# Kernel optimization log

Measured on AMD Instinct MI355X. Metric: run time of the kernel, lower is better.

The kernel has to match this reference:

```python
import jax, jax.numpy as jnp
import numpy as np

B, S, HID = 2, 2048, 2048
H, KVH, D = 32, 4, 128
EPS = 1e-6
ROPE_THETA = 1e6
INIT = 0.02


def setup_inputs() -> dict:
    key = jax.random.key(0)
    ks = jax.random.split(key, 6)
    hidden_states = jax.random.normal(ks[0], (B, S, HID), jnp.float32)
    q_w = jax.random.normal(ks[1], (HID, H * D), jnp.float32) * INIT
    k_w = jax.random.normal(ks[2], (HID, KVH * D), jnp.float32) * INIT
    v_w = jax.random.normal(ks[3], (HID, KVH * D), jnp.float32) * INIT
    o_w = jax.random.normal(ks[4], (H * D, HID), jnp.float32) * INIT
    q_norm_w = jnp.ones((D,), jnp.float32)
    k_norm_w = jnp.ones((D,), jnp.float32)
    # rotary embeddings, computed once per position (B, S, D)
    pos = jnp.arange(S, dtype=jnp.float32)
    inv_freq = 1.0 / (ROPE_THETA ** (jnp.arange(0, D, 2, dtype=jnp.float32) / D))
    freqs = pos[:, None] * inv_freq[None, :]          # (S, D/2)
    emb = jnp.concatenate([freqs, freqs], axis=-1)    # (S, D)
    cos = jnp.broadcast_to(jnp.cos(emb)[None], (B, S, D))
    sin = jnp.broadcast_to(jnp.sin(emb)[None], (B, S, D))
    # causal mask (is_causal=True, sliding_window=None)
    attn_mask = jnp.tril(jnp.ones((S, S), bool))[None, None]  # (1,1,S,S)
    return {"hidden_states": hidden_states, "cos": cos, "sin": sin,
            "q_w": q_w, "k_w": k_w, "v_w": v_w, "o_w": o_w,
            "q_norm_w": q_norm_w, "k_norm_w": k_norm_w, "attn_mask": attn_mask}


def _rms_norm(x, w):
    xf = x.astype(jnp.float32)
    var = jnp.mean(jax.lax.square(xf), axis=-1, keepdims=True)
    return (w * (xf * jax.lax.rsqrt(var + EPS))).astype(x.dtype)


def _rotate_half(x):
    x1, x2 = jnp.split(x, 2, axis=-1)
    return jnp.concatenate([-x2, x1], axis=-1)


def _apply_rope(q, k, cos, sin):
    # q: (B,H,S,D), k: (B,KVH,S,D); cos/sin: (B,S,D) -> (B,1,S,D)
    cos = cos[:, None]
    sin = sin[:, None]
    q = q * cos + _rotate_half(q) * sin
    k = k * cos + _rotate_half(k) * sin
    return q, k


def reference(hidden_states, cos, sin, q_w, k_w, v_w, o_w, q_norm_w, k_norm_w, attn_mask):
    b, s, _ = hidden_states.shape
    scaling = D ** (-0.5)
    # projections + per-head QK RMSNorm
    q = _rms_norm((hidden_states @ q_w).reshape(b, s, H, D), q_norm_w)
    k = _rms_norm((hidden_states @ k_w).reshape(b, s, KVH, D), k_norm_w)
    v = (hidden_states @ v_w).reshape(b, s, KVH, D)
    q = jnp.transpose(q, (0, 2, 1, 3))   # (b,H,s,D)
    k = jnp.transpose(k, (0, 2, 1, 3))   # (b,KVH,s,D)
    v = jnp.transpose(v, (0, 2, 1, 3))
    q, k = _apply_rope(q, k, cos, sin)
    # GQA: repeat KV heads across groups
    groups = H // KVH
    k = jnp.repeat(k, groups, axis=1)    # (b,H,s,D)
    v = jnp.repeat(v, groups, axis=1)
    # eager softmax attention (fp32 softmax)
    scores = jnp.einsum('bhqd,bhkd->bhqk', q, k).astype(jnp.float32) * scaling
    scores = jnp.where(attn_mask, scores, jnp.float32(-1e30))
    probs = jax.nn.softmax(scores, axis=-1).astype(q.dtype)
    attn = jnp.einsum('bhqk,bhkd->bhqd', probs, v)
    attn = jnp.transpose(attn, (0, 2, 1, 3)).reshape(b, s, H * D)
    return attn @ o_w
```

## Files before the change

### kernel.cpp

```cpp
#include <hip/hip_runtime.h>
#include <hip/hip_bf16.h>

typedef unsigned short u16;
typedef __attribute__((ext_vector_type(4))) float f32x4;
typedef __attribute__((ext_vector_type(16))) float f32x16;
typedef __attribute__((ext_vector_type(8))) short bf16x8;
typedef __attribute__((ext_vector_type(4))) unsigned u32x4;

#define B_ 2
#define S_ 2048
#define HID_ 2048
#define H_ 32
#define KVH_ 4
#define D_ 128
#define M_ 4096
#define NQ_ 4096
#define NKV_ 512

typedef const __attribute__((address_space(1))) void gconst_void;
typedef __attribute__((address_space(3))) void lds_void;

static __device__ __forceinline__ void gload_lds16(const void* g, void* l) {
  __builtin_amdgcn_global_load_lds((gconst_void*)g, (lds_void*)l, 16, 0, 0);
}

#define WAITV(N) asm volatile("s_waitcnt vmcnt(" #N ")" ::: "memory")
#define WAITL0() asm volatile("s_waitcnt lgkmcnt(0)" ::: "memory")
#define SBAR() __builtin_amdgcn_s_barrier()
#define SCHED0() __builtin_amdgcn_sched_barrier(0)
#define CFENCE() asm volatile("" ::: "memory")

static __device__ __forceinline__ u16 f2b(float f) {
  union { float f; unsigned i; } x; x.f = f;
  return (u16)((x.i + 0x7fffu + ((x.i >> 16) & 1u)) >> 16);
}
static __device__ __forceinline__ float b2f(u16 u) {
  union { unsigned i; float f; } x; x.i = ((unsigned)u) << 16;
  return x.f;
}
static __device__ __forceinline__ float max3f(float a, float b, float c) {
  float d;
  asm("v_max3_f32 %0, %1, %2, %3" : "=v"(d) : "v"(a), "v"(b), "v"(c));
  return d;
}

static __device__ __forceinline__ void tr_tile(const float* __restrict__ W,
    u16* __restrict__ Wt, int K, int N, int n0, int k0, u16 (*t)[72]) {
  int tid = threadIdx.x;
  int r = tid >> 4;
  int c4 = (tid & 15) * 4;
#pragma unroll
  for (int i = 0; i < 4; i++) {
    int k = r + i * 16;
    float4 v = *reinterpret_cast<const float4*>(W + (size_t)(k0 + k) * N + n0 + c4);
    t[k][c4 + 0] = f2b(v.x); t[k][c4 + 1] = f2b(v.y);
    t[k][c4 + 2] = f2b(v.z); t[k][c4 + 3] = f2b(v.w);
  }
  __syncthreads();
#pragma unroll
  for (int i = 0; i < 4; i++) {
    int n = r + i * 16;
    ushort4 o;
    o.x = t[c4 + 0][n]; o.y = t[c4 + 1][n]; o.z = t[c4 + 2][n]; o.w = t[c4 + 3][n];
    *reinterpret_cast<ushort4*>(Wt + (size_t)(n0 + n) * K + k0 + c4) = o;
  }
}

__global__ __launch_bounds__(256) void k_prep(const float* __restrict__ hidden, u16* __restrict__ hb,
    const float* __restrict__ qw, u16* __restrict__ qwt,
    const float* __restrict__ kw, u16* __restrict__ kwt,
    const float* __restrict__ vw, u16* __restrict__ vwt,
    const float* __restrict__ ow, u16* __restrict__ owt) {
  __shared__ u16 t[64][72];
  const int bid = blockIdx.x;
  if (bid < 2048) {
    const int n4 = M_ * HID_ / 4;
    int i = bid * 256 + threadIdx.x;
    const int stride = 2048 * 256;
    for (; i < n4; i += stride) {
      float4 v = reinterpret_cast<const float4*>(hidden)[i];
      ushort4 o;
      o.x = f2b(v.x); o.y = f2b(v.y); o.z = f2b(v.z); o.w = f2b(v.w);
      reinterpret_cast<ushort4*>(hb)[i] = o;
    }
  } else if (bid < 4096) {
    int l = bid - 2048;
    tr_tile(qw, qwt, HID_, NQ_, (l & 63) * 64, (l >> 6) * 64, t);
  } else if (bid < 4352) {
    int l = bid - 4096;
    tr_tile(kw, kwt, HID_, NKV_, (l & 7) * 64, (l >> 3) * 64, t);
  } else if (bid < 4608) {
    int l = bid - 4352;
    tr_tile(vw, vwt, HID_, NKV_, (l & 7) * 64, (l >> 3) * 64, t);
  } else {
    int l = bid - 4608;
    tr_tile(ow, owt, NQ_, HID_, (l & 31) * 64, (l >> 5) * 64, t);
  }
}

__device__ __forceinline__ void gemm_core(const u16* __restrict__ A, const u16* __restrict__ Bt,
                                          int K, int m0, int n0,
                                          u16* As, u16* Bs, f32x4 (&acc)[4][4]) {
  const int tid = threadIdx.x;
  const int lane = tid & 63;
  const int wid = tid >> 6;
  const int wr = wid >> 1, wc = wid & 1;
  const int lrow = lane & 15;
  const int hi = lane >> 4;
  const f32x4 zz = {0.f, 0.f, 0.f, 0.f};
#pragma unroll
  for (int i = 0; i < 4; i++)
#pragma unroll
    for (int j = 0; j < 4; j++) acc[i][j] = zz;

  const int srow = tid >> 3;
  const int sc16 = tid & 7;
  const int nk = K >> 6;
  int cur = 0;

#pragma unroll
  for (int rep = 0; rep < 4; rep++) {
    int row = rep * 32 + srow;
    int gcol = ((sc16 ^ (row & 7)) << 3);
    gload_lds16(A + (size_t)(m0 + row) * K + gcol, As + row * 64 + sc16 * 8);
    gload_lds16(Bt + (size_t)(n0 + row) * K + gcol, Bs + row * 64 + sc16 * 8);
  }

  for (int t = 0; t < nk; t++) {
    if (t + 1 < nk) {
      int nxt = cur ^ 1;
      int kb = (t + 1) << 6;
#pragma unroll
      for (int rep = 0; rep < 4; rep++) {
        int row = rep * 32 + srow;
        int gcol = kb + ((sc16 ^ (row & 7)) << 3);
        gload_lds16(A + (size_t)(m0 + row) * K + gcol, As + nxt * 8192 + row * 64 + sc16 * 8);
        gload_lds16(Bt + (size_t)(n0 + row) * K + gcol, Bs + nxt * 8192 + row * 64 + sc16 * 8);
      }
      WAITV(8);
    } else {
      WAITV(0);
    }
    SCHED0(); SBAR(); CFENCE(); SCHED0();

    const u16* Ac = As + cur * 8192;
    const u16* Bc = Bs + cur * 8192;
#pragma unroll
    for (int kc = 0; kc < 2; kc++) {
      bf16x8 af[4], bfr[4];
#pragma unroll
      for (int i = 0; i < 4; i++) {
        int row = wr * 64 + i * 16 + lrow;
        af[i] = *reinterpret_cast<const bf16x8*>(Ac + row * 64 + ((((kc << 2) + hi) ^ (row & 7)) << 3));
      }
#pragma unroll
      for (int j = 0; j < 4; j++) {
        int row = wc * 64 + j * 16 + lrow;
        bfr[j] = *reinterpret_cast<const bf16x8*>(Bc + row * 64 + ((((kc << 2) + hi) ^ (row & 7)) << 3));
      }
#pragma unroll
      for (int i = 0; i < 4; i++)
#pragma unroll
        for (int j = 0; j < 4; j++)
          acc[i][j] = __builtin_amdgcn_mfma_f32_16x16x32_bf16(af[i], bfr[j], acc[i][j], 0, 0, 0);
    }
    SBAR(); SCHED0();
    cur ^= 1;
  }
}

__global__ __launch_bounds__(512, 2) void k_gemm_q8(const u16* __restrict__ A,
    const u16* __restrict__ Bt, u16* __restrict__ qb) {
  __shared__ u16 Ash[2][2][128 * 64];
  __shared__ u16 Bsh[2][2][128 * 64];
  const int bid = blockIdx.x;
  const int wg = (bid & 7) * 32 + (bid >> 3);
  const int mt = wg & 15, nt = wg >> 4;
  const int m0 = mt * 256, n0 = nt * 256;
  const int K = HID_, nk = K >> 6;
  const int tid = threadIdx.x, lane = tid & 63;
  const int wv = tid >> 6, wr = wv >> 2, wc = wv & 3;
  const int lrow = lane & 15, hi4 = lane >> 4;

  const int s0r = tid >> 3, sc = tid & 7;
  const int s1r = (tid + 512) >> 3;

  auto stgA = [&](int h, int t, int d) {
    gload_lds16(A + (size_t)(m0 + h * 128 + s0r) * K + t * 64 + ((sc ^ (s0r & 7)) << 3),
                &Ash[d][h][s0r * 64 + sc * 8]);
    gload_lds16(A + (size_t)(m0 + h * 128 + s1r) * K + t * 64 + ((sc ^ (s1r & 7)) << 3),
                &Ash[d][h][s1r * 64 + sc * 8]);
  };
  auto stgB = [&](int h, int t, int d) {
    gload_lds16(Bt + (size_t)(n0 + h * 128 + s0r) * K + t * 64 + ((sc ^ (s0r & 7)) << 3),
                &Bsh[d][h][s0r * 64 + sc * 8]);
    gload_lds16(Bt + (size_t)(n0 + h * 128 + s1r) * K + t * 64 + ((sc ^ (s1r & 7)) << 3),
                &Bsh[d][h][s1r * 64 + sc * 8]);
  };

  f32x4 acc[8][4];
  const f32x4 zz = {0.f, 0.f, 0.f, 0.f};
#pragma unroll
  for (int f = 0; f < 8; f++)
#pragma unroll
    for (int j = 0; j < 4; j++) acc[f][j] = zz;

  bf16x8 af0[4][2], af1[4][2], bfr[2][2];

  auto lda = [&](bf16x8 (&dst)[4][2], int mh, int d) {
#pragma unroll
    for (int fi = 0; fi < 4; fi++) {
      int row = fi * 32 + wr * 16 + lrow;
#pragma unroll
      for (int kk = 0; kk < 2; kk++)
        dst[fi][kk] = *reinterpret_cast<const bf16x8*>(
            &Ash[d][mh][row * 64 + ((((kk << 2) + hi4) ^ (row & 7)) << 3)]);
    }
  };
  auto ldb = [&](int nh, int d) {
#pragma unroll
    for (int ji = 0; ji < 2; ji++) {
      int row = ji * 64 + wc * 16 + lrow;
#pragma unroll
      for (int kk = 0; kk < 2; kk++)
        bfr[ji][kk] = *reinterpret_cast<const bf16x8*>(
            &Bsh[d][nh][row * 64 + ((((kk << 2) + hi4) ^ (row & 7)) << 3)]);
    }
  };
  auto mq = [&](bf16x8 (&afh)[4][2], int mh, int nh) {
    __builtin_amdgcn_s_setprio(1);
#pragma unroll
    for (int kk = 0; kk < 2; kk++)
#pragma unroll
      for (int fi = 0; fi < 4; fi++)
#pragma unroll
        for (int ji = 0; ji < 2; ji++)
          acc[mh * 4 + fi][nh * 2 + ji] = __builtin_amdgcn_mfma_f32_16x16x32_bf16(
              afh[fi][kk], bfr[ji][kk], acc[mh * 4 + fi][nh * 2 + ji], 0, 0, 0);
    __builtin_amdgcn_s_setprio(0);
  };

  stgA(0, 0, 0); stgA(1, 0, 0); stgB(0, 0, 0); stgB(1, 0, 0);
  WAITV(2); SCHED0();
  SBAR(); SCHED0();

  for (int t = 0; t < nk; t++) {
    const int d = t & 1, nd = d ^ 1;
    const bool pre = (t + 1 < nk);
    lda(af0, 0, d); ldb(0, d);
    if (pre) stgA(0, t + 1, nd);
    SCHED0(); SBAR();
    WAITL0(); SCHED0();
    mq(af0, 0, 0);
    SBAR(); SCHED0();
    lda(af1, 1, d);
    if (pre) stgA(1, t + 1, nd);
    WAITV(4); SCHED0(); SBAR();
    WAITL0(); SCHED0();
    mq(af1, 1, 0);
    SBAR(); SCHED0();
    ldb(1, d);
    if (pre) stgB(0, t + 1, nd);
    SCHED0(); SBAR();
    WAITL0(); SCHED0();
    mq(af1, 1, 1);
    SBAR(); SCHED0();
    if (pre) stgB(1, t + 1, nd);
    WAITV(2); SCHED0(); SBAR();
    mq(af0, 0, 1);
    SBAR(); SCHED0();
  }

  const int lr4 = hi4 * 4, lc = lane & 15;
#pragma unroll
  for (int f = 0; f < 8; f++)
#pragma unroll
    for (int j = 0; j < 4; j++)
#pragma unroll
      for (int rr = 0; rr < 4; rr++) {
        int m = m0 + f * 32 + wr * 16 + lr4 + rr;
        int ncol = n0 + j * 64 + wc * 16 + lc;
        int b = m >> 11, s = m & (S_ - 1);
        int head = ncol >> 7, dd = ncol & 127;
        qb[(((size_t)b * H_ + head) * S_ + s) * D_ + dd] = f2b(acc[f][j][rr]);
      }
}

__global__ __launch_bounds__(256, 2) void k_gemm_kv(const u16* __restrict__ hb,
    const u16* __restrict__ kwt, const u16* __restrict__ vwt,
    u16* __restrict__ kb, u16* __restrict__ vb) {
  __shared__ u16 As[2 * 128 * 64], Bs[2 * 128 * 64];
  const int bid = blockIdx.x;
  const int wg = (bid & 7) * 32 + (bid >> 3);
  const int mt = wg & 31, nt = wg >> 5;
  const bool isv = nt >= 4;
  const int head = isv ? nt - 4 : nt;
  const u16* Bt = isv ? vwt : kwt;
  f32x4 acc[4][4];
  gemm_core(hb, Bt, HID_, mt * 128, head * 128, As, Bs, acc);
  const int lane = threadIdx.x & 63;
  const int wid = threadIdx.x >> 6;
  const int wr = wid >> 1, wc = wid & 1;
  const int lr4 = (lane >> 4) * 4, lc = lane & 15;
#pragma unroll
  for (int i = 0; i < 4; i++)
#pragma unroll
    for (int j = 0; j < 4; j++)
#pragma unroll
      for (int r = 0; r < 4; r++) {
        int m = mt * 128 + wr * 64 + i * 16 + lr4 + r;
        int d = wc * 64 + j * 16 + lc;
        int b = m >> 11, s = m & (S_ - 1);
        u16 val = f2b(acc[i][j][r]);
        if (isv) vb[(((size_t)b * KVH_ + head) * D_ + d) * S_ + s] = val;
        else     kb[(((size_t)b * KVH_ + head) * S_ + s) * D_ + d] = val;
      }
}

__global__ __launch_bounds__(256, 2) void k_gemm_o(const u16* __restrict__ ab,
    const u16* __restrict__ owt, float* __restrict__ out) {
  __shared__ u16 As[2 * 128 * 64], Bs[2 * 128 * 64];
  const int bid = blockIdx.x;
  const int wg = (bid & 7) * 64 + (bid >> 3);
  const int mt = wg & 31, nt = wg >> 5;
  f32x4 acc[4][4];
  gemm_core(ab, owt, NQ_, mt * 128, nt * 128, As, Bs, acc);
  const int lane = threadIdx.x & 63;
  const int wid = threadIdx.x >> 6;
  const int wr = wid >> 1, wc = wid & 1;
  const int lr4 = (lane >> 4) * 4, lc = lane & 15;
#pragma unroll
  for (int i = 0; i < 4; i++)
#pragma unroll
    for (int j = 0; j < 4; j++)
#pragma unroll
      for (int r = 0; r < 4; r++) {
        int m = mt * 128 + wr * 64 + i * 16 + lr4 + r;
        int n = nt * 128 + wc * 64 + j * 16 + lc;
        out[(size_t)m * HID_ + n] = acc[i][j][r];
      }
}

__global__ __launch_bounds__(256) void k_norm_rope(u16* __restrict__ qb, u16* __restrict__ kb,
    const float* __restrict__ cosp, const float* __restrict__ sinp,
    const float* __restrict__ qnw, const float* __restrict__ knw) {
  int row = blockIdx.x * 4 + (threadIdx.x >> 6);
  int lane = threadIdx.x & 63;
  const int QROWS = B_ * H_ * S_;
  u16* ptr; const float* nw; int b, s; float os;
  if (row < QROWS) {
    ptr = qb + (size_t)row * D_; nw = qnw;
    s = row & (S_ - 1); b = row / (H_ * S_);
    os = 0.08838834764831845f * 1.44269504088896340f;
  } else {
    int r2 = row - QROWS;
    ptr = kb + (size_t)r2 * D_; nw = knw;
    s = r2 & (S_ - 1); b = r2 / (KVH_ * S_);
    os = 1.0f;
  }
  int d = lane * 2;
  float x0 = b2f(ptr[d]), x1 = b2f(ptr[d + 1]);
  float ss = x0 * x0 + x1 * x1;
#pragma unroll
  for (int m = 1; m < 64; m <<= 1) ss += __shfl_xor(ss, m);
  float inv = rsqrtf(ss * (1.0f / 128.0f) + 1e-6f) * os;
  x0 = x0 * inv * nw[d]; x1 = x1 * inv * nw[d + 1];
  float p0 = __shfl_xor(x0, 32), p1 = __shfl_xor(x1, 32);
  float r0 = (lane < 32) ? -p0 : p0;
  float r1 = (lane < 32) ? -p1 : p1;
  const float* cp = cosp + ((size_t)b * S_ + s) * D_;
  const float* sp = sinp + ((size_t)b * S_ + s) * D_;
  ptr[d]     = f2b(x0 * cp[d]     + r0 * sp[d]);
  ptr[d + 1] = f2b(x1 * cp[d + 1] + r1 * sp[d + 1]);
}

__global__ __launch_bounds__(256, 2) void k_attn(const u16* __restrict__ q,
    const u16* __restrict__ k, const u16* __restrict__ vt, u16* __restrict__ out) {
  __shared__ u16 Kb[2 * 64 * 128];
  __shared__ u16 Vb[128 * 64];
  const int bid = blockIdx.x;
  const int wg = (bid & 7) * 64 + (bid >> 3);
  const int qx = wg & 7, bh = wg >> 3;
  const int b = bh >> 5, h = bh & 31;
  const int kvh = h >> 3;
  const int tid = threadIdx.x, lane = tid & 63, w = tid >> 6;
  const int lq = lane & 31, hi = lane >> 5;
  const u16* qp  = q  + ((size_t)(b * H_ + h) * S_) * D_;
  const u16* kp  = k  + ((size_t)(b * KVH_ + kvh) * S_) * D_;
  const u16* vtp = vt + ((size_t)(b * KVH_ + kvh) * D_) * S_;

  const int rowKa = tid >> 4;
  const int colK  = ((tid & 15) ^ (rowKa & 15)) << 3;
  const int rowVa = tid >> 3;
  const int colV  = ((tid & 7) ^ (rowVa & 7)) << 3;

  auto stageK = [&](int n0, int cu) {
    u16* kd = Kb + cu * 8192 + tid * 8;
#pragma unroll
    for (int p = 0; p < 4; p++)
      gload_lds16(kp + (size_t)(n0 + p * 16 + rowKa) * D_ + colK, kd + p * 2048);
  };
  auto stageV = [&](int n0) {
    u16* vd = Vb + tid * 8;
#pragma unroll
    for (int p = 0; p < 4; p++)
      gload_lds16(vtp + (size_t)(p * 32 + rowVa) * S_ + n0 + colV, vd + p * 2048);
  };

  const f32x16 z16 = {0.f};
  int cur = 0;

  for (int half = 0; half < 2; half++) {
    const int qt = half ? (15 - qx) : qx;
    const int q0 = qt * 128;
    const int last = 2 * qt + 1;
    const int qg = q0 + 32 * w + lq;

    SBAR(); SCHED0();
    stageK(0, cur);
    stageV(0);

    bf16x8 qf[8];
#pragma unroll
    for (int ds = 0; ds < 8; ds++)
      qf[ds] = *reinterpret_cast<const bf16x8*>(qp + (size_t)qg * D_ + ds * 16 + hi * 8);

    f32x16 oacc[4];
#pragma unroll
    for (int dt = 0; dt < 4; dt++) oacc[dt] = z16;
    float mrun = -1e30f, lrun = 0.f;

    for (int nt = 0; nt <= last; nt++) {
      const int n0 = nt * 64;
      if (nt < last) {
        stageK(n0 + 64, cur ^ 1);
        WAITV(8);
      } else {
        WAITV(4);
      }
      SCHED0(); SBAR(); CFENCE(); SCHED0();

      const u16* Kc = Kb + cur * 8192;
      const bool skip = (n0 > q0 + 32 * w + 31);

      f32x16 sacc[2];
      if (!skip) {
        const bool needmask = (n0 + 63 > q0 + 32 * w);

        sacc[0] = z16; sacc[1] = z16;
#pragma unroll
        for (int ds = 0; ds < 8; ds++) {
          const int sl = (((ds << 1) + hi) ^ (lq & 15)) << 3;
          bf16x8 ka0 = *reinterpret_cast<const bf16x8*>(Kc + lq * 128 + sl);
          bf16x8 ka1 = *reinterpret_cast<const bf16x8*>(Kc + (lq + 32) * 128 + sl);
          __builtin_amdgcn_s_setprio(1);
          sacc[0] = __builtin_amdgcn_mfma_f32_32x32x16_bf16(ka0, qf[ds], sacc[0], 0, 0, 0);
          sacc[1] = __builtin_amdgcn_mfma_f32_32x32x16_bf16(ka1, qf[ds], sacc[1], 0, 0, 0);
          __builtin_amdgcn_s_setprio(0);
        }

        if (needmask) {
#pragma unroll
          for (int t = 0; t < 2; t++)
#pragma unroll
            for (int r = 0; r < 16; r++) {
              int kvg = n0 + 32 * t + (r & 3) + 8 * (r >> 2) + 4 * hi;
              if (kvg > qg) sacc[t][r] = -1e30f;
            }
        }
        float tm = fmaxf(sacc[0][0], sacc[0][1]);
#pragma unroll
        for (int i = 1; i < 16; i++) {
          const int e0 = 2 * i, e1 = 2 * i + 1;
          tm = max3f(tm, sacc[e0 >> 4][e0 & 15], sacc[e1 >> 4][e1 & 15]);
        }
        tm = fmaxf(tm, __shfl_xor(tm, 32));
        if (__any(tm > mrun + 8.f)) {
          float mn = fmaxf(mrun, tm);
          float al = exp2f(mrun - mn);
          mrun = mn;
          lrun *= al;
#pragma unroll
          for (int r = 0; r < 16; r++) {
            float ar = __shfl(al, (r & 3) + 8 * (r >> 2) + 4 * hi);
#pragma unroll
            for (int dt = 0; dt < 4; dt++) oacc[dt][r] *= ar;
          }
        }
        float rs = 0.f;
#pragma unroll
        for (int t = 0; t < 2; t++)
#pragma unroll
          for (int r = 0; r < 16; r++) {
            float pv = exp2f(sacc[t][r] - mrun);
            sacc[t][r] = pv;
            rs += pv;
          }
        rs += __shfl_xor(rs, 32);
        lrun += rs;
      }

      if (nt < last) WAITV(4); else WAITV(0);
      SCHED0(); SBAR(); CFENCE(); SCHED0();

      if (!skip) {
        u32x4 pa[4];
#pragma unroll
        for (int t = 0; t < 2; t++)
#pragma unroll
          for (int ksl = 0; ksl < 2; ksl++) {
            unsigned wa, wb, wc2, wd;
            asm("v_cvt_pk_bf16_f32 %0, %1, %2" : "=v"(wa)
                : "v"(sacc[t][8 * ksl + 0]), "v"(sacc[t][8 * ksl + 1]));
            asm("v_cvt_pk_bf16_f32 %0, %1, %2" : "=v"(wb)
                : "v"(sacc[t][8 * ksl + 2]), "v"(sacc[t][8 * ksl + 3]));
            asm("v_cvt_pk_bf16_f32 %0, %1, %2" : "=v"(wc2)
                : "v"(sacc[t][8 * ksl + 4]), "v"(sacc[t][8 * ksl + 5]));
            asm("v_cvt_pk_bf16_f32 %0, %1, %2" : "=v"(wd)
                : "v"(sacc[t][8 * ksl + 6]), "v"(sacc[t][8 * ksl + 7]));
            asm("v_permlane32_swap_b32 %0, %1" : "+v"(wa), "+v"(wc2));
            asm("v_permlane32_swap_b32 %0, %1" : "+v"(wb), "+v"(wd));
            u32x4 t4 = {wa, wb, wc2, wd};
            pa[t * 2 + ksl] = t4;
          }

#pragma unroll
        for (int ks = 0; ks < 4; ks++) {
          bf16x8 paf = __builtin_bit_cast(bf16x8, pa[ks]);
          bf16x8 bv[4];
#pragma unroll
          for (int dt = 0; dt < 4; dt++) {
            int rowv = dt * 32 + lq;
            bv[dt] = *reinterpret_cast<const bf16x8*>(
                Vb + rowv * 64 + ((((ks << 1) + hi) ^ (rowv & 7)) << 3));
          }
          __builtin_amdgcn_s_setprio(1);
#pragma unroll
          for (int dt = 0; dt < 4; dt++)
            oacc[dt] = __builtin_amdgcn_mfma_f32_32x32x16_bf16(paf, bv[dt], oacc[dt], 0, 0, 0);
          __builtin_amdgcn_s_setprio(0);
        }
      }

      if (nt < last) {
        SBAR(); SCHED0();
        stageV(nt * 64 + 64);
      }
      cur ^= 1;
    }

    float linv = 1.0f / lrun;
#pragma unroll
    for (int r = 0; r < 16; r++) {
      const int idx_r = (r & 3) + 8 * (r >> 2) + 4 * hi;
      float lr = __shfl(linv, idx_r);
      size_t base = ((size_t)b * S_ + (q0 + 32 * w + idx_r)) * NQ_ + h * D_ + lq;
#pragma unroll
      for (int dt = 0; dt < 4; dt++)
        out[base + dt * 32] = f2b(oacc[dt][r] * lr);
    }
  }
}

extern "C" void kernel_launch(void* const* d_in, const int* in_sizes, int n_in,
                              void* d_out, int out_size, void* d_ws, size_t ws_size,
                              hipStream_t stream) {
  const float* hidden = (const float*)d_in[0];
  const float* cosp   = (const float*)d_in[1];
  const float* sinp   = (const float*)d_in[2];
  const float* q_w    = (const float*)d_in[3];
  const float* k_w    = (const float*)d_in[4];
  const float* v_w    = (const float*)d_in[5];
  const float* o_w    = (const float*)d_in[6];
  const float* qnw    = (const float*)d_in[7];
  const float* knw    = (const float*)d_in[8];

  char* p = (char*)d_ws;
  u16* hb  = (u16*)p; p += (size_t)M_ * HID_ * 2;
  u16* qwt = (u16*)p; p += (size_t)NQ_ * HID_ * 2;
  u16* kwt = (u16*)p; p += (size_t)NKV_ * HID_ * 2;
  u16* vwt = (u16*)p; p += (size_t)NKV_ * HID_ * 2;
  u16* owt = (u16*)p; p += (size_t)HID_ * NQ_ * 2;
  u16* qb  = (u16*)p; p += (size_t)B_ * H_ * S_ * D_ * 2;
  u16* kb  = (u16*)p; p += (size_t)B_ * KVH_ * S_ * D_ * 2;
  u16* vb  = (u16*)p; p += (size_t)B_ * KVH_ * S_ * D_ * 2;
  u16* ab  = (u16*)p; p += (size_t)M_ * NQ_ * 2;

  k_prep<<<6656, 256, 0, stream>>>(hidden, hb, q_w, qwt, k_w, kwt, v_w, vwt, o_w, owt);
  k_gemm_q8<<<256, 512, 0, stream>>>(hb, qwt, qb);
  k_gemm_kv<<<256, 256, 0, stream>>>(hb, kwt, vwt, kb, vb);
  k_norm_rope<<<(B_ * H_ * S_ + B_ * KVH_ * S_) / 4, 256, 0, stream>>>(qb, kb, cosp, sinp, qnw, knw);
  k_attn<<<512, 256, 0, stream>>>(qb, kb, vb, ab);
  k_gemm_o<<<512, 256, 0, stream>>>(ab, owt, (float*)d_out);
}
```

Baseline: 319.0 us.

## Use 256x128 8-wave O-projection GEMM and one query tile per attention block

Replaces the 128x128 O-projection GEMM with a 512-thread kernel that computes 256x128 tiles, double-buffers A and B through LDS and splits the A tile into two halves to overlap loads with 16x16x32 MFMAs. The attention kernel drops its paired-tile loop, where each block handled a short and a long causal query tile. It now launches 1024 blocks with one tile each, heaviest tiles first. This gives more parallelism and relies on the hardware scheduler for load balance instead of manual pairing. The risks are more blocks and a longer tail if the largest tiles do not spread evenly across CUs.

```diff
diff --git a/kernel.cpp b/kernel.cpp
--- a/kernel.cpp
+++ b/kernel.cpp
@@ -317,27 +317,107 @@
       }
 }
 
-__global__ __launch_bounds__(256, 2) void k_gemm_o(const u16* __restrict__ ab,
-    const u16* __restrict__ owt, float* __restrict__ out) {
-  __shared__ u16 As[2 * 128 * 64], Bs[2 * 128 * 64];
+__global__ __launch_bounds__(512, 2) void k_gemm_o8(const u16* __restrict__ A,
+    const u16* __restrict__ Bt, float* __restrict__ out) {
+  __shared__ u16 Ash[2][2][128 * 64];
+  __shared__ u16 Bsh[2][128 * 64];
   const int bid = blockIdx.x;
-  const int wg = (bid & 7) * 64 + (bid >> 3);
-  const int mt = wg & 31, nt = wg >> 5;
-  f32x4 acc[4][4];
-  gemm_core(ab, owt, NQ_, mt * 128, nt * 128, As, Bs, acc);
-  const int lane = threadIdx.x & 63;
-  const int wid = threadIdx.x >> 6;
-  const int wr = wid >> 1, wc = wid & 1;
-  const int lr4 = (lane >> 4) * 4, lc = lane & 15;
-#pragma unroll
-  for (int i = 0; i < 4; i++)
-#pragma unroll
-    for (int j = 0; j < 4; j++)
-#pragma unroll
-      for (int r = 0; r < 4; r++) {
-        int m = mt * 128 + wr * 64 + i * 16 + lr4 + r;
-        int n = nt * 128 + wc * 64 + j * 16 + lc;
-        out[(size_t)m * HID_ + n] = acc[i][j][r];
+  const int wg = (bid & 7) * 32 + (bid >> 3);
+  const int mt = wg & 15, nt = wg >> 4;
+  const int m0 = mt * 256, n0 = nt * 128;
+  const int K = NQ_, nk = K >> 6;
+  const int tid = threadIdx.x, lane = tid & 63;
+  const int wv = tid >> 6, wr = wv >> 2, wc = wv & 3;
+  const int lrow = lane & 15, hi4 = lane >> 4;
+
+  const int s0r = tid >> 3, sc = tid & 7;
+  const int s1r = (tid + 512) >> 3;
+
+  auto stgA = [&](int h, int t, int d) {
+    gload_lds16(A + (size_t)(m0 + h * 128 + s0r) * K + t * 64 + ((sc ^ (s0r & 7)) << 3),
+                &Ash[d][h][s0r * 64 + sc * 8]);
+    gload_lds16(A + (size_t)(m0 + h * 128 + s1r) * K + t * 64 + ((sc ^ (s1r & 7)) << 3),
+                &Ash[d][h][s1r * 64 + sc * 8]);
+  };
+  auto stgB = [&](int t, int d) {
+    gload_lds16(Bt + (size_t)(n0 + s0r) * K + t * 64 + ((sc ^ (s0r & 7)) << 3),
+                &Bsh[d][s0r * 64 + sc * 8]);
+    gload_lds16(Bt + (size_t)(n0 + s1r) * K + t * 64 + ((sc ^ (s1r & 7)) << 3),
+                &Bsh[d][s1r * 64 + sc * 8]);
+  };
+
+  f32x4 acc[8][2];
+  const f32x4 zz = {0.f, 0.f, 0.f, 0.f};
+#pragma unroll
+  for (int f = 0; f < 8; f++) { acc[f][0] = zz; acc[f][1] = zz; }
+
+  bf16x8 af0[4][2], af1[4][2], bfr[2][2];
+
+  auto lda = [&](bf16x8 (&dst)[4][2], int mh, int d) {
+#pragma unroll
+    for (int fi = 0; fi < 4; fi++) {
+      int row = fi * 32 + wr * 16 + lrow;
+#pragma unroll
+      for (int kk = 0; kk < 2; kk++)
+        dst[fi][kk] = *reinterpret_cast<const bf16x8*>(
+            &Ash[d][mh][row * 64 + ((((kk << 2) + hi4) ^ (row & 7)) << 3)]);
+    }
+  };
+  auto ldb = [&](int d) {
+#pragma unroll
+    for (int ji = 0; ji < 2; ji++) {
+      int row = ji * 64 + wc * 16 + lrow;
+#pragma unroll
+      for (int kk = 0; kk < 2; kk++)
+        bfr[ji][kk] = *reinterpret_cast<const bf16x8*>(
+            &Bsh[d][row * 64 + ((((kk << 2) + hi4) ^ (row & 7)) << 3)]);
+    }
+  };
+  auto mq = [&](bf16x8 (&afh)[4][2], int mh) {
+    __builtin_amdgcn_s_setprio(1);
+#pragma unroll
+    for (int kk = 0; kk < 2; kk++)
+#pragma unroll
+      for (int fi = 0; fi < 4; fi++)
+#pragma unroll
+        for (int ji = 0; ji < 2; ji++)
+          acc[mh * 4 + fi][ji] = __builtin_amdgcn_mfma_f32_16x16x32_bf16(
+              afh[fi][kk], bfr[ji][kk], acc[mh * 4 + fi][ji], 0, 0, 0);
+    __builtin_amdgcn_s_setprio(0);
+  };
+
+  stgA(0, 0, 0); stgB(0, 0); stgA(1, 0, 0);
+  WAITV(2); SCHED0();
+  SBAR(); SCHED0();
+
+  for (int t = 0; t < nk; t++) {
+    const int d = t & 1, nd = d ^ 1;
+    const bool pre = (t + 1 < nk);
+    lda(af0, 0, d); ldb(d);
+    if (pre) { stgA(0, t + 1, nd); WAITV(2); } else { WAITV(0); }
+    SCHED0(); SBAR();
+    WAITL0(); SCHED0();
+    mq(af0, 0);
+    SBAR(); SCHED0();
+    lda(af1, 1, d);
+    if (pre) { stgB(t + 1, nd); stgA(1, t + 1, nd); WAITV(4); }
+    SCHED0(); SBAR();
+    WAITL0(); SCHED0();
+    mq(af1, 1);
+    if (pre) WAITV(2);
+    SCHED0(); SBAR(); SCHED0();
+  }
+
+  const int lr4 = hi4 * 4, lc = lane & 15;
+#pragma unroll
+  for (int f = 0; f < 8; f++)
+#pragma unroll
+    for (int j = 0; j < 2; j++)
+#pragma unroll
+      for (int rr = 0; rr < 4; rr++) {
+        int m = m0 + f * 32 + wr * 16 + lr4 + rr;
+        int n = n0 + j * 64 + wc * 16 + lc;
+        out[(size_t)m * HID_ + n] = acc[f][j][rr];
       }
 }
 
@@ -379,8 +459,9 @@
   __shared__ u16 Kb[2 * 64 * 128];
   __shared__ u16 Vb[128 * 64];
   const int bid = blockIdx.x;
-  const int wg = (bid & 7) * 64 + (bid >> 3);
-  const int qx = wg & 7, bh = wg >> 3;
+  const int wg = (bid & 7) * 128 + (bid >> 3);
+  const int qt = 15 - (wg & 15);
+  const int bh = wg >> 4;
   const int b = bh >> 5, h = bh & 31;
   const int kvh = h >> 3;
   const int tid = threadIdx.x, lane = tid & 63, w = tid >> 6;
@@ -408,157 +489,152 @@
   };
 
   const f32x16 z16 = {0.f};
+  const int q0 = qt * 128;
+  const int last = 2 * qt + 1;
+  const int qg = q0 + 32 * w + lq;
   int cur = 0;
 
-  for (int half = 0; half < 2; half++) {
-    const int qt = half ? (15 - qx) : qx;
-    const int q0 = qt * 128;
-    const int last = 2 * qt + 1;
-    const int qg = q0 + 32 * w + lq;
-
-    SBAR(); SCHED0();
-    stageK(0, cur);
-    stageV(0);
-
-    bf16x8 qf[8];
-#pragma unroll
-    for (int ds = 0; ds < 8; ds++)
-      qf[ds] = *reinterpret_cast<const bf16x8*>(qp + (size_t)qg * D_ + ds * 16 + hi * 8);
-
-    f32x16 oacc[4];
-#pragma unroll
-    for (int dt = 0; dt < 4; dt++) oacc[dt] = z16;
-    float mrun = -1e30f, lrun = 0.f;
-
-    for (int nt = 0; nt <= last; nt++) {
-      const int n0 = nt * 64;
-      if (nt < last) {
-        stageK(n0 + 64, cur ^ 1);
-        WAITV(8);
-      } else {
-        WAITV(4);
-      }
-      SCHED0(); SBAR(); CFENCE(); SCHED0();
-
-      const u16* Kc = Kb + cur * 8192;
-      const bool skip = (n0 > q0 + 32 * w + 31);
-
-      f32x16 sacc[2];
-      if (!skip) {
-        const bool needmask = (n0 + 63 > q0 + 32 * w);
-
-        sacc[0] = z16; sacc[1] = z16;
-#pragma unroll
-        for (int ds = 0; ds < 8; ds++) {
-          const int sl = (((ds << 1) + hi) ^ (lq & 15)) << 3;
-          bf16x8 ka0 = *reinterpret_cast<const bf16x8*>(Kc + lq * 128 + sl);
-          bf16x8 ka1 = *reinterpret_cast<const bf16x8*>(Kc + (lq + 32) * 128 + sl);
-          __builtin_amdgcn_s_setprio(1);
-          sacc[0] = __builtin_amdgcn_mfma_f32_32x32x16_bf16(ka0, qf[ds], sacc[0], 0, 0, 0);
-          sacc[1] = __builtin_amdgcn_mfma_f32_32x32x16_bf16(ka1, qf[ds], sacc[1], 0, 0, 0);
-          __builtin_amdgcn_s_setprio(0);
+  stageK(0, 0);
+  stageV(0);
+
+  bf16x8 qf[8];
+#pragma unroll
+  for (int ds = 0; ds < 8; ds++)
+    qf[ds] = *reinterpret_cast<const bf16x8*>(qp + (size_t)qg * D_ + ds * 16 + hi * 8);
+
+  f32x16 oacc[4];
+#pragma unroll
+  for (int dt = 0; dt < 4; dt++) oacc[dt] = z16;
+  float mrun = -1e30f, lrun = 0.f;
+
+  for (int nt = 0; nt <= last; nt++) {
+    const int n0 = nt * 64;
+    if (nt < last) {
+      stageK(n0 + 64, cur ^ 1);
+      WAITV(8);
+    } else {
+      WAITV(4);
+    }
+    SCHED0(); SBAR(); CFENCE(); SCHED0();
+
+    const u16* Kc = Kb + cur * 8192;
+    const bool skip = (n0 > q0 + 32 * w + 31);
+
+    f32x16 sacc[2];
+    if (!skip) {
+      const bool needmask = (n0 + 63 > q0 + 32 * w);
+
+      sacc[0] = z16; sacc[1] = z16;
+#pragma unroll
+      for (int ds = 0; ds < 8; ds++) {
+        const int sl = (((ds << 1) + hi) ^ (lq & 15)) << 3;
+        bf16x8 ka0 = *reinterpret_cast<const bf16x8*>(Kc + lq * 128 + sl);
+        bf16x8 ka1 = *reinterpret_cast<const bf16x8*>(Kc + (lq + 32) * 128 + sl);
+        __builtin_amdgcn_s_setprio(1);
+        sacc[0] = __builtin_amdgcn_mfma_f32_32x32x16_bf16(ka0, qf[ds], sacc[0], 0, 0, 0);
+        sacc[1] = __builtin_amdgcn_mfma_f32_32x32x16_bf16(ka1, qf[ds], sacc[1], 0, 0, 0);
+        __builtin_amdgcn_s_setprio(0);
+      }
+
+      if (needmask) {
+#pragma unroll
+        for (int t = 0; t < 2; t++)
+#pragma unroll
+          for (int r = 0; r < 16; r++) {
+            int kvg = n0 + 32 * t + (r & 3) + 8 * (r >> 2) + 4 * hi;
+            if (kvg > qg) sacc[t][r] = -1e30f;
+          }
+      }
+      float tm = fmaxf(sacc[0][0], sacc[0][1]);
+#pragma unroll
+      for (int i = 1; i < 16; i++) {
+        const int e0 = 2 * i, e1 = 2 * i + 1;
+        tm = max3f(tm, sacc[e0 >> 4][e0 & 15], sacc[e1 >> 4][e1 & 15]);
+      }
+      tm = fmaxf(tm, __shfl_xor(tm, 32));
+      if (__any(tm > mrun + 8.f)) {
+        float mn = fmaxf(mrun, tm);
+        float al = exp2f(mrun - mn);
+        mrun = mn;
+        lrun *= al;
+#pragma unroll
+        for (int r = 0; r < 16; r++) {
+          float ar = __shfl(al, (r & 3) + 8 * (r >> 2) + 4 * hi);
+#pragma unroll
+          for (int dt = 0; dt < 4; dt++) oacc[dt][r] *= ar;
         }
-
-        if (needmask) {
-#pragma unroll
-          for (int t = 0; t < 2; t++)
-#pragma unroll
-            for (int r = 0; r < 16; r++) {
-              int kvg = n0 + 32 * t + (r & 3) + 8 * (r >> 2) + 4 * hi;
-              if (kvg > qg) sacc[t][r] = -1e30f;
-            }
+      }
+      float rs = 0.f;
+#pragma unroll
+      for (int t = 0; t < 2; t++)
+#pragma unroll
+        for (int r = 0; r < 16; r++) {
+          float pv = exp2f(sacc[t][r] - mrun);
+          sacc[t][r] = pv;
+          rs += pv;
         }
-        float tm = fmaxf(sacc[0][0], sacc[0][1]);
-#pragma unroll
-        for (int i = 1; i < 16; i++) {
-          const int e0 = 2 * i, e1 = 2 * i + 1;
-          tm = max3f(tm, sacc[e0 >> 4][e0 & 15], sacc[e1 >> 4][e1 & 15]);
+      rs += __shfl_xor(rs, 32);
+      lrun += rs;
+    }
+
+    if (nt < last) WAITV(4); else WAITV(0);
+    SCHED0(); SBAR(); CFENCE(); SCHED0();
+
+    if (!skip) {
+      u32x4 pa[4];
+#pragma unroll
+      for (int t = 0; t < 2; t++)
+#pragma unroll
+        for (int ksl = 0; ksl < 2; ksl++) {
+          unsigned wa, wb, wc2, wd;
+          asm("v_cvt_pk_bf16_f32 %0, %1, %2" : "=v"(wa)
+              : "v"(sacc[t][8 * ksl + 0]), "v"(sacc[t][8 * ksl + 1]));
+          asm("v_cvt_pk_bf16_f32 %0, %1, %2" : "=v"(wb)
+              : "v"(sacc[t][8 * ksl + 2]), "v"(sacc[t][8 * ksl + 3]));
+          asm("v_cvt_pk_bf16_f32 %0, %1, %2" : "=v"(wc2)
+              : "v"(sacc[t][8 * ksl + 4]), "v"(sacc[t][8 * ksl + 5]));
+          asm("v_cvt_pk_bf16_f32 %0, %1, %2" : "=v"(wd)
+              : "v"(sacc[t][8 * ksl + 6]), "v"(sacc[t][8 * ksl + 7]));
+          asm("v_permlane32_swap_b32 %0, %1" : "+v"(wa), "+v"(wc2));
+          asm("v_permlane32_swap_b32 %0, %1" : "+v"(wb), "+v"(wd));
+          u32x4 t4 = {wa, wb, wc2, wd};
+          pa[t * 2 + ksl] = t4;
         }
-        tm = fmaxf(tm, __shfl_xor(tm, 32));
-        if (__any(tm > mrun + 8.f)) {
-          float mn = fmaxf(mrun, tm);
-          float al = exp2f(mrun - mn);
-          mrun = mn;
-          lrun *= al;
-#pragma unroll
-          for (int r = 0; r < 16; r++) {
-            float ar = __shfl(al, (r & 3) + 8 * (r >> 2) + 4 * hi);
-#pragma unroll
-            for (int dt = 0; dt < 4; dt++) oacc[dt][r] *= ar;
-          }
+
+#pragma unroll
+      for (int ks = 0; ks < 4; ks++) {
+        bf16x8 paf = __builtin_bit_cast(bf16x8, pa[ks]);
+        bf16x8 bv[4];
+#pragma unroll
+        for (int dt = 0; dt < 4; dt++) {
+          int rowv = dt * 32 + lq;
+          bv[dt] = *reinterpret_cast<const bf16x8*>(
+              Vb + rowv * 64 + ((((ks << 1) + hi) ^ (rowv & 7)) << 3));
         }
-        float rs = 0.f;
-#pragma unroll
-        for (int t = 0; t < 2; t++)
-#pragma unroll
-          for (int r = 0; r < 16; r++) {
-            float pv = exp2f(sacc[t][r] - mrun);
-            sacc[t][r] = pv;
-            rs += pv;
-          }
-        rs += __shfl_xor(rs, 32);
-        lrun += rs;
-      }
-
-      if (nt < last) WAITV(4); else WAITV(0);
-      SCHED0(); SBAR(); CFENCE(); SCHED0();
-
-      if (!skip) {
-        u32x4 pa[4];
-#pragma unroll
-        for (int t = 0; t < 2; t++)
-#pragma unroll
-          for (int ksl = 0; ksl < 2; ksl++) {
-            unsigned wa, wb, wc2, wd;
-            asm("v_cvt_pk_bf16_f32 %0, %1, %2" : "=v"(wa)
-                : "v"(sacc[t][8 * ksl + 0]), "v"(sacc[t][8 * ksl + 1]));
-            asm("v_cvt_pk_bf16_f32 %0, %1, %2" : "=v"(wb)
-                : "v"(sacc[t][8 * ksl + 2]), "v"(sacc[t][8 * ksl + 3]));
-            asm("v_cvt_pk_bf16_f32 %0, %1, %2" : "=v"(wc2)
-                : "v"(sacc[t][8 * ksl + 4]), "v"(sacc[t][8 * ksl + 5]));
-            asm("v_cvt_pk_bf16_f32 %0, %1, %2" : "=v"(wd)
-                : "v"(sacc[t][8 * ksl + 6]), "v"(sacc[t][8 * ksl + 7]));
-            asm("v_permlane32_swap_b32 %0, %1" : "+v"(wa), "+v"(wc2));
-            asm("v_permlane32_swap_b32 %0, %1" : "+v"(wb), "+v"(wd));
-            u32x4 t4 = {wa, wb, wc2, wd};
-            pa[t * 2 + ksl] = t4;
-          }
-
-#pragma unroll
-        for (int ks = 0; ks < 4; ks++) {
-          bf16x8 paf = __builtin_bit_cast(bf16x8, pa[ks]);
-          bf16x8 bv[4];
-#pragma unroll
-          for (int dt = 0; dt < 4; dt++) {
-            int rowv = dt * 32 + lq;
-            bv[dt] = *reinterpret_cast<const bf16x8*>(
-                Vb + rowv * 64 + ((((ks << 1) + hi) ^ (rowv & 7)) << 3));
-          }
-          __builtin_amdgcn_s_setprio(1);
-#pragma unroll
-          for (int dt = 0; dt < 4; dt++)
-            oacc[dt] = __builtin_amdgcn_mfma_f32_32x32x16_bf16(paf, bv[dt], oacc[dt], 0, 0, 0);
-          __builtin_amdgcn_s_setprio(0);
-        }
-      }
-
-      if (nt < last) {
-        SBAR(); SCHED0();
-        stageV(nt * 64 + 64);
-      }
-      cur ^= 1;
-    }
-
-    float linv = 1.0f / lrun;
-#pragma unroll
-    for (int r = 0; r < 16; r++) {
-      const int idx_r = (r & 3) + 8 * (r >> 2) + 4 * hi;
-      float lr = __shfl(linv, idx_r);
-      size_t base = ((size_t)b * S_ + (q0 + 32 * w + idx_r)) * NQ_ + h * D_ + lq;
-#pragma unroll
-      for (int dt = 0; dt < 4; dt++)
-        out[base + dt * 32] = f2b(oacc[dt][r] * lr);
-    }
+        __builtin_amdgcn_s_setprio(1);
+#pragma unroll
+        for (int dt = 0; dt < 4; dt++)
+          oacc[dt] = __builtin_amdgcn_mfma_f32_32x32x16_bf16(paf, bv[dt], oacc[dt], 0, 0, 0);
+        __builtin_amdgcn_s_setprio(0);
+      }
+    }
+
+    if (nt < last) {
+      SBAR(); SCHED0();
+      stageV(nt * 64 + 64);
+    }
+    cur ^= 1;
+  }
+
+  float linv = 1.0f / lrun;
+#pragma unroll
+  for (int r = 0; r < 16; r++) {
+    const int idx_r = (r & 3) + 8 * (r >> 2) + 4 * hi;
+    float lr = __shfl(linv, idx_r);
+    size_t base = ((size_t)b * S_ + (q0 + 32 * w + idx_r)) * NQ_ + h * D_ + lq;
+#pragma unroll
+    for (int dt = 0; dt < 4; dt++)
+      out[base + dt * 32] = f2b(oacc[dt][r] * lr);
   }
 }
 
@@ -590,6 +666,6 @@
   k_gemm_q8<<<256, 512, 0, stream>>>(hb, qwt, qb);
   k_gemm_kv<<<256, 256, 0, stream>>>(hb, kwt, vwt, kb, vb);
   k_norm_rope<<<(B_ * H_ * S_ + B_ * KVH_ * S_) / 4, 256, 0, stream>>>(qb, kb, cosp, sinp, qnw, knw);
-  k_attn<<<512, 256, 0, stream>>>(qb, kb, vb, ab);
-  k_gemm_o<<<512, 256, 0, stream>>>(ab, owt, (float*)d_out);
-}
+  k_attn<<<1024, 256, 0, stream>>>(qb, kb, vb, ab);
+  k_gemm_o8<<<256, 512, 0, stream>>>(ab, owt, (float*)d_out);
+}
```

Measured after the change: 376.6 us. +18.1%, slower.

## Split causal attention KV range across two workgroups with split-K merge kernel

Applied to the files above, without the earlier changes.

Doubles the attention grid so each (batch, head, q-pair) gets two workgroups that each process exactly 17 KV tiles. Group 0 finishes the short low query tile and then starts the high tile, while group 1 handles the rest of the high tile. The two partial outputs and their max/sum statistics go to scratch buffers reused from dead workspace, and a new merge kernel combines them. This is meant to balance work and raise parallelism, at the cost of an extra launch, round-tripping partials through memory, and bf16 rounding of the partial outputs.

```diff
diff --git a/kernel.cpp b/kernel.cpp
--- a/kernel.cpp
+++ b/kernel.cpp
@@ -375,14 +375,18 @@
 }
 
 __global__ __launch_bounds__(256, 2) void k_attn(const u16* __restrict__ q,
-    const u16* __restrict__ k, const u16* __restrict__ vt, u16* __restrict__ out) {
+    const u16* __restrict__ k, const u16* __restrict__ vt, u16* __restrict__ out,
+    u16* __restrict__ pO0, u16* __restrict__ pO1, float* __restrict__ pML) {
   __shared__ u16 Kb[2 * 64 * 128];
   __shared__ u16 Vb[128 * 64];
   const int bid = blockIdx.x;
-  const int wg = (bid & 7) * 64 + (bid >> 3);
-  const int qx = wg & 7, bh = wg >> 3;
-  const int b = bh >> 5, h = bh & 31;
-  const int kvh = h >> 3;
+  const int wg = (bid & 7) * 128 + (bid >> 3);
+  const int qx = wg & 7, g = (wg >> 3) & 1, bh = wg >> 4;
+  const int b = bh >> 5, h = bh & 31, kvh = h >> 3;
+  const int qtH = 15 - qx;
+  const int L0 = 2 * qx + 2;
+  const int H0 = 15 - 2 * qx;
+  const int slot = bh * 8 + (qtH - 8);
   const int tid = threadIdx.x, lane = tid & 63, w = tid >> 6;
   const int lq = lane & 31, hi = lane >> 5;
   const u16* qp  = q  + ((size_t)(b * H_ + h) * S_) * D_;
@@ -394,6 +398,10 @@
   const int rowVa = tid >> 3;
   const int colV  = ((tid & 7) ^ (rowVa & 7)) << 3;
 
+  auto kvoff = [&](int i) {
+    if (g == 0) return ((i < L0) ? i : (i - L0)) * 64;
+    return (H0 + i) * 64;
+  };
   auto stageK = [&](int n0, int cu) {
     u16* kd = Kb + cu * 8192 + tid * 8;
 #pragma unroll
@@ -408,158 +416,222 @@
   };
 
   const f32x16 z16 = {0.f};
+  int q0 = (g == 0) ? qx * 128 : qtH * 128;
   int cur = 0;
 
-  for (int half = 0; half < 2; half++) {
-    const int qt = half ? (15 - qx) : qx;
-    const int q0 = qt * 128;
-    const int last = 2 * qt + 1;
+  stageK(kvoff(0), 0);
+  stageV(kvoff(0));
+
+  bf16x8 qf[8];
+#pragma unroll
+  for (int ds = 0; ds < 8; ds++)
+    qf[ds] = *reinterpret_cast<const bf16x8*>(qp + (size_t)(q0 + 32 * w + lq) * D_ + ds * 16 + hi * 8);
+
+  f32x16 oacc[4];
+#pragma unroll
+  for (int dt = 0; dt < 4; dt++) oacc[dt] = z16;
+  float mrun = -1e30f, lrun = 0.f;
+
+  for (int i = 0; i < 17; i++) {
+    if (i < 16) {
+      stageK(kvoff(i + 1), cur ^ 1);
+      WAITV(8);
+    } else {
+      WAITV(4);
+    }
+    SCHED0(); SBAR(); CFENCE(); SCHED0();
+
+    if (g == 0 && i == L0) {
+      float linv = 1.0f / lrun;
+#pragma unroll
+      for (int r = 0; r < 16; r++) {
+        const int idx_r = (r & 3) + 8 * (r >> 2) + 4 * hi;
+        float lr = __shfl(linv, idx_r);
+        size_t base = ((size_t)b * S_ + (q0 + 32 * w + idx_r)) * NQ_ + h * D_ + lq;
+#pragma unroll
+        for (int dt = 0; dt < 4; dt++)
+          out[base + dt * 32] = f2b(oacc[dt][r] * lr);
+      }
+#pragma unroll
+      for (int dt = 0; dt < 4; dt++) oacc[dt] = z16;
+      mrun = -1e30f; lrun = 0.f;
+      q0 = qtH * 128;
+#pragma unroll
+      for (int ds = 0; ds < 8; ds++)
+        qf[ds] = *reinterpret_cast<const bf16x8*>(
+            qp + (size_t)(q0 + 32 * w + lq) * D_ + ds * 16 + hi * 8);
+    }
+
+    const int n0 = kvoff(i);
     const int qg = q0 + 32 * w + lq;
-
-    SBAR(); SCHED0();
-    stageK(0, cur);
-    stageV(0);
-
-    bf16x8 qf[8];
-#pragma unroll
-    for (int ds = 0; ds < 8; ds++)
-      qf[ds] = *reinterpret_cast<const bf16x8*>(qp + (size_t)qg * D_ + ds * 16 + hi * 8);
-
-    f32x16 oacc[4];
-#pragma unroll
-    for (int dt = 0; dt < 4; dt++) oacc[dt] = z16;
-    float mrun = -1e30f, lrun = 0.f;
-
-    for (int nt = 0; nt <= last; nt++) {
-      const int n0 = nt * 64;
-      if (nt < last) {
-        stageK(n0 + 64, cur ^ 1);
-        WAITV(8);
-      } else {
-        WAITV(4);
-      }
-      SCHED0(); SBAR(); CFENCE(); SCHED0();
-
-      const u16* Kc = Kb + cur * 8192;
-      const bool skip = (n0 > q0 + 32 * w + 31);
-
-      f32x16 sacc[2];
-      if (!skip) {
-        const bool needmask = (n0 + 63 > q0 + 32 * w);
-
-        sacc[0] = z16; sacc[1] = z16;
-#pragma unroll
-        for (int ds = 0; ds < 8; ds++) {
-          const int sl = (((ds << 1) + hi) ^ (lq & 15)) << 3;
-          bf16x8 ka0 = *reinterpret_cast<const bf16x8*>(Kc + lq * 128 + sl);
-          bf16x8 ka1 = *reinterpret_cast<const bf16x8*>(Kc + (lq + 32) * 128 + sl);
-          __builtin_amdgcn_s_setprio(1);
-          sacc[0] = __builtin_amdgcn_mfma_f32_32x32x16_bf16(ka0, qf[ds], sacc[0], 0, 0, 0);
-          sacc[1] = __builtin_amdgcn_mfma_f32_32x32x16_bf16(ka1, qf[ds], sacc[1], 0, 0, 0);
-          __builtin_amdgcn_s_setprio(0);
+    const u16* Kc = Kb + cur * 8192;
+    const bool skip = (n0 > q0 + 32 * w + 31);
+
+    f32x16 sacc[2];
+    if (!skip) {
+      const bool needmask = (n0 + 63 > q0 + 32 * w);
+
+      sacc[0] = z16; sacc[1] = z16;
+#pragma unroll
+      for (int ds = 0; ds < 8; ds++) {
+        const int sl = (((ds << 1) + hi) ^ (lq & 15)) << 3;
+        bf16x8 ka0 = *reinterpret_cast<const bf16x8*>(Kc + lq * 128 + sl);
+        bf16x8 ka1 = *reinterpret_cast<const bf16x8*>(Kc + (lq + 32) * 128 + sl);
+        __builtin_amdgcn_s_setprio(1);
+        sacc[0] = __builtin_amdgcn_mfma_f32_32x32x16_bf16(ka0, qf[ds], sacc[0], 0, 0, 0);
+        sacc[1] = __builtin_amdgcn_mfma_f32_32x32x16_bf16(ka1, qf[ds], sacc[1], 0, 0, 0);
+        __builtin_amdgcn_s_setprio(0);
+      }
+
+      if (needmask) {
+#pragma unroll
+        for (int t = 0; t < 2; t++)
+#pragma unroll
+          for (int r = 0; r < 16; r++) {
+            int kvg = n0 + 32 * t + (r & 3) + 8 * (r >> 2) + 4 * hi;
+            if (kvg > qg) sacc[t][r] = -1e30f;
+          }
+      }
+      float tm = fmaxf(sacc[0][0], sacc[0][1]);
+#pragma unroll
+      for (int i2 = 1; i2 < 16; i2++) {
+        const int e0 = 2 * i2, e1 = 2 * i2 + 1;
+        tm = max3f(tm, sacc[e0 >> 4][e0 & 15], sacc[e1 >> 4][e1 & 15]);
+      }
+      tm = fmaxf(tm, __shfl_xor(tm, 32));
+      if (__any(tm > mrun + 8.f)) {
+        float mn = fmaxf(mrun, tm);
+        float al = exp2f(mrun - mn);
+        mrun = mn;
+        lrun *= al;
+#pragma unroll
+        for (int r = 0; r < 16; r++) {
+          float ar = __shfl(al, (r & 3) + 8 * (r >> 2) + 4 * hi);
+#pragma unroll
+          for (int dt = 0; dt < 4; dt++) oacc[dt][r] *= ar;
         }
-
-        if (needmask) {
-#pragma unroll
-          for (int t = 0; t < 2; t++)
-#pragma unroll
-            for (int r = 0; r < 16; r++) {
-              int kvg = n0 + 32 * t + (r & 3) + 8 * (r >> 2) + 4 * hi;
-              if (kvg > qg) sacc[t][r] = -1e30f;
-            }
+      }
+      float rs = 0.f;
+#pragma unroll
+      for (int t = 0; t < 2; t++)
+#pragma unroll
+        for (int r = 0; r < 16; r++) {
+          float pv = exp2f(sacc[t][r] - mrun);
+          sacc[t][r] = pv;
+          rs += pv;
         }
-        float tm = fmaxf(sacc[0][0], sacc[0][1]);
-#pragma unroll
-        for (int i = 1; i < 16; i++) {
-          const int e0 = 2 * i, e1 = 2 * i + 1;
-          tm = max3f(tm, sacc[e0 >> 4][e0 & 15], sacc[e1 >> 4][e1 & 15]);
+      rs += __shfl_xor(rs, 32);
+      lrun += rs;
+    }
+
+    if (i < 16) WAITV(4); else WAITV(0);
+    SCHED0(); SBAR(); CFENCE(); SCHED0();
+
+    if (!skip) {
+      u32x4 pa[4];
+#pragma unroll
+      for (int t = 0; t < 2; t++)
+#pragma unroll
+        for (int ksl = 0; ksl < 2; ksl++) {
+          unsigned wa, wb, wc2, wd;
+          asm("v_cvt_pk_bf16_f32 %0, %1, %2" : "=v"(wa)
+              : "v"(sacc[t][8 * ksl + 0]), "v"(sacc[t][8 * ksl + 1]));
+          asm("v_cvt_pk_bf16_f32 %0, %1, %2" : "=v"(wb)
+              : "v"(sacc[t][8 * ksl + 2]), "v"(sacc[t][8 * ksl + 3]));
+          asm("v_cvt_pk_bf16_f32 %0, %1, %2" : "=v"(wc2)
+              : "v"(sacc[t][8 * ksl + 4]), "v"(sacc[t][8 * ksl + 5]));
+          asm("v_cvt_pk_bf16_f32 %0, %1, %2" : "=v"(wd)
+              : "v"(sacc[t][8 * ksl + 6]), "v"(sacc[t][8 * ksl + 7]));
+          asm("v_permlane32_swap_b32 %0, %1" : "+v"(wa), "+v"(wc2));
+          asm("v_permlane32_swap_b32 %0, %1" : "+v"(wb), "+v"(wd));
+          u32x4 t4 = {wa, wb, wc2, wd};
+          pa[t * 2 + ksl] = t4;
         }
-        tm = fmaxf(tm, __shfl_xor(tm, 32));
-        if (__any(tm > mrun + 8.f)) {
-          float mn = fmaxf(mrun, tm);
-          float al = exp2f(mrun - mn);
-          mrun = mn;
-          lrun *= al;
-#pragma unroll
-          for (int r = 0; r < 16; r++) {
-            float ar = __shfl(al, (r & 3) + 8 * (r >> 2) + 4 * hi);
-#pragma unroll
-            for (int dt = 0; dt < 4; dt++) oacc[dt][r] *= ar;
-          }
+
+#pragma unroll
+      for (int ks = 0; ks < 4; ks++) {
+        bf16x8 paf = __builtin_bit_cast(bf16x8, pa[ks]);
+        bf16x8 bv[4];
+#pragma unroll
+        for (int dt = 0; dt < 4; dt++) {
+          int rowv = dt * 32 + lq;
+          bv[dt] = *reinterpret_cast<const bf16x8*>(
+              Vb + rowv * 64 + ((((ks << 1) + hi) ^ (rowv & 7)) << 3));
         }
-        float rs = 0.f;
-#pragma unroll
-        for (int t = 0; t < 2; t++)
-#pragma unroll
-          for (int r = 0; r < 16; r++) {
-            float pv = exp2f(sacc[t][r] - mrun);
-            sacc[t][r] = pv;
-            rs += pv;
-          }
-        rs += __shfl_xor(rs, 32);
-        lrun += rs;
-      }
-
-      if (nt < last) WAITV(4); else WAITV(0);
-      SCHED0(); SBAR(); CFENCE(); SCHED0();
-
-      if (!skip) {
-        u32x4 pa[4];
-#pragma unroll
-        for (int t = 0; t < 2; t++)
-#pragma unroll
-          for (int ksl = 0; ksl < 2; ksl++) {
-            unsigned wa, wb, wc2, wd;
-            asm("v_cvt_pk_bf16_f32 %0, %1, %2" : "=v"(wa)
-                : "v"(sacc[t][8 * ksl + 0]), "v"(sacc[t][8 * ksl + 1]));
-            asm("v_cvt_pk_bf16_f32 %0, %1, %2" : "=v"(wb)
-                : "v"(sacc[t][8 * ksl + 2]), "v"(sacc[t][8 * ksl + 3]));
-            asm("v_cvt_pk_bf16_f32 %0, %1, %2" : "=v"(wc2)
-                : "v"(sacc[t][8 * ksl + 4]), "v"(sacc[t][8 * ksl + 5]));
-            asm("v_cvt_pk_bf16_f32 %0, %1, %2" : "=v"(wd)
-                : "v"(sacc[t][8 * ksl + 6]), "v"(sacc[t][8 * ksl + 7]));
-            asm("v_permlane32_swap_b32 %0, %1" : "+v"(wa), "+v"(wc2));
-            asm("v_permlane32_swap_b32 %0, %1" : "+v"(wb), "+v"(wd));
-            u32x4 t4 = {wa, wb, wc2, wd};
-            pa[t * 2 + ksl] = t4;
-          }
-
-#pragma unroll
-        for (int ks = 0; ks < 4; ks++) {
-          bf16x8 paf = __builtin_bit_cast(bf16x8, pa[ks]);
-          bf16x8 bv[4];
-#pragma unroll
-          for (int dt = 0; dt < 4; dt++) {
-            int rowv = dt * 32 + lq;
-            bv[dt] = *reinterpret_cast<const bf16x8*>(
-                Vb + rowv * 64 + ((((ks << 1) + hi) ^ (rowv & 7)) << 3));
-          }
-          __builtin_amdgcn_s_setprio(1);
-#pragma unroll
-          for (int dt = 0; dt < 4; dt++)
-            oacc[dt] = __builtin_amdgcn_mfma_f32_32x32x16_bf16(paf, bv[dt], oacc[dt], 0, 0, 0);
-          __builtin_amdgcn_s_setprio(0);
-        }
-      }
-
-      if (nt < last) {
-        SBAR(); SCHED0();
-        stageV(nt * 64 + 64);
-      }
-      cur ^= 1;
-    }
-
-    float linv = 1.0f / lrun;
-#pragma unroll
-    for (int r = 0; r < 16; r++) {
-      const int idx_r = (r & 3) + 8 * (r >> 2) + 4 * hi;
-      float lr = __shfl(linv, idx_r);
-      size_t base = ((size_t)b * S_ + (q0 + 32 * w + idx_r)) * NQ_ + h * D_ + lq;
-#pragma unroll
-      for (int dt = 0; dt < 4; dt++)
-        out[base + dt * 32] = f2b(oacc[dt][r] * lr);
-    }
-  }
+        __builtin_amdgcn_s_setprio(1);
+#pragma unroll
+        for (int dt = 0; dt < 4; dt++)
+          oacc[dt] = __builtin_amdgcn_mfma_f32_32x32x16_bf16(paf, bv[dt], oacc[dt], 0, 0, 0);
+        __builtin_amdgcn_s_setprio(0);
+      }
+    }
+
+    if (i < 16) {
+      SBAR(); SCHED0();
+      stageV(kvoff(i + 1));
+    }
+    cur ^= 1;
+  }
+
+  {
+    unsigned* o32 = (unsigned*)(g ? pO1 : pO0) + (size_t)slot * 8192;
+#pragma unroll
+    for (int dt = 0; dt < 4; dt++)
+#pragma unroll
+      for (int r = 0; r < 16; r += 2) {
+        unsigned pk;
+        asm("v_cvt_pk_bf16_f32 %0, %1, %2" : "=v"(pk)
+            : "v"(oacc[dt][r]), "v"(oacc[dt][r + 1]));
+        int rowb = 32 * w + (r & 3) + 8 * (r >> 2) + 4 * hi;
+        o32[(dt * 32 + lq) * 64 + (rowb >> 1)] = pk;
+      }
+    if (hi == 0) {
+      float* pml = pML + (size_t)(g * 512 + slot) * 256;
+      pml[32 * w + lq] = mrun;
+      pml[128 + 32 * w + lq] = lrun;
+    }
+  }
+}
+
+__global__ __launch_bounds__(256) void k_merge(const u16* __restrict__ pO0,
+    const u16* __restrict__ pO1, const float* __restrict__ pML, u16* __restrict__ out) {
+  __shared__ u16 t[128 * 128];
+  const int slot = blockIdx.x;
+  const int bh = slot >> 3, qtH = (slot & 7) + 8;
+  const int b = bh >> 5, h = bh & 31;
+  const int q0 = qtH * 128;
+  const int tid = threadIdx.x;
+  const unsigned* o0 = (const unsigned*)pO0 + (size_t)slot * 8192;
+  const unsigned* o1 = (const unsigned*)pO1 + (size_t)slot * 8192;
+  const float* ml0 = pML + (size_t)slot * 256;
+  const float* ml1 = pML + (size_t)(512 + slot) * 256;
+
+  const int p = tid & 63, dg = tid >> 6;
+  const int r0 = 2 * p, r1 = 2 * p + 1;
+  float m0a = ml0[r0], m1a = ml1[r0];
+  float ma = fmaxf(m0a, m1a);
+  float a0a = exp2f(m0a - ma), a1a = exp2f(m1a - ma);
+  float lia = 1.0f / (ml0[128 + r0] * a0a + ml1[128 + r0] * a1a);
+  float m0b = ml0[r1], m1b = ml1[r1];
+  float mb = fmaxf(m0b, m1b);
+  float a0b = exp2f(m0b - mb), a1b = exp2f(m1b - mb);
+  float lib = 1.0f / (ml0[128 + r1] * a0b + ml1[128 + r1] * a1b);
+#pragma unroll
+  for (int dd = 0; dd < 32; dd++) {
+    int d = dg * 32 + dd;
+    unsigned u0 = o0[d * 64 + p], u1 = o1[d * 64 + p];
+    float va = (b2f((u16)(u0 & 0xffffu)) * a0a + b2f((u16)(u1 & 0xffffu)) * a1a) * lia;
+    float vb = (b2f((u16)(u0 >> 16)) * a0b + b2f((u16)(u1 >> 16)) * a1b) * lib;
+    t[r0 * 128 + d] = f2b(va);
+    t[r1 * 128 + d] = f2b(vb);
+  }
+  __syncthreads();
+  const int row = tid >> 1, half = tid & 1;
+  u16* dst = out + ((size_t)b * S_ + q0 + row) * NQ_ + h * D_ + half * 64;
+  const u16* src = t + row * 128 + half * 64;
+#pragma unroll
+  for (int c = 0; c < 8; c++)
+    *reinterpret_cast<bf16x8*>(dst + c * 8) = *reinterpret_cast<const bf16x8*>(src + c * 8);
 }
 
 extern "C" void kernel_launch(void* const* d_in, const int* in_sizes, int n_in,
@@ -590,6 +662,7 @@
   k_gemm_q8<<<256, 512, 0, stream>>>(hb, qwt, qb);
   k_gemm_kv<<<256, 256, 0, stream>>>(hb, kwt, vwt, kb, vb);
   k_norm_rope<<<(B_ * H_ * S_ + B_ * KVH_ * S_) / 4, 256, 0, stream>>>(qb, kb, cosp, sinp, qnw, knw);
-  k_attn<<<512, 256, 0, stream>>>(qb, kb, vb, ab);
+  k_attn<<<1024, 256, 0, stream>>>(qb, kb, vb, ab, qwt, hb, (float*)kwt);
+  k_merge<<<512, 256, 0, stream>>>(qwt, hb, (float*)kwt, ab);
   k_gemm_o<<<512, 256, 0, stream>>>(ab, owt, (float*)d_out);
 }
```

New measurement: 345.4 us. 8.3% more time.
